# Kernel optimization log

Measured on AMD Instinct MI355X. Metric: run time of the kernel, lower is better.

## Reference

```python
import jax, jax.numpy as jnp
import numpy as np


def setup_inputs() -> dict:
    key = jax.random.key(0)
    k1, k2, k3, k4, k5 = jax.random.split(key, 5)
    B, S, T = 256, 512, 64
    emissions = jax.random.normal(k1, (B, S, T), dtype=jnp.float32)
    tags = jax.random.randint(k2, (B, S), 0, T, dtype=jnp.int64)
    mask = jnp.ones((B, S), dtype=jnp.int32)
    init_range = 0.1
    start_transitions = jax.random.uniform(k3, (T,), minval=-init_range, maxval=init_range, dtype=jnp.float32)
    end_transitions = jax.random.uniform(k4, (T,), minval=-init_range, maxval=init_range, dtype=jnp.float32)
    transitions = jax.random.uniform(k5, (T, T), minval=-init_range, maxval=init_range, dtype=jnp.float32)
    return {"emissions": emissions, "tags": tags, "mask": mask,
            "start_transitions": start_transitions,
            "end_transitions": end_transitions,
            "transitions": transitions}


def _crf_nll_mean(emissions, tags, mask, start_transitions, end_transitions, transitions):
    # batch_first -> time-major: [S, B, T], [S, B]
    em = jnp.transpose(emissions, (1, 0, 2))
    tg = jnp.transpose(tags, (1, 0))
    mk = jnp.transpose(mask, (1, 0))
    maskf = mk.astype(em.dtype)                      # [S, B]
    S, B, T = em.shape
    batch_idx = jnp.arange(B)

    # ---- numerator: score of the gold path (fully vectorized) ----
    emit = jnp.take_along_axis(em, tg[:, :, None], axis=2)[..., 0]   # [S, B]
    trans_sc = transitions[tg[:-1], tg[1:]]                          # [S-1, B]
    score_num = start_transitions[tg[0]] + emit[0]
    score_num = score_num + jnp.sum((trans_sc + emit[1:]) * maskf[1:], axis=0)
    seq_ends = jnp.sum(mk, axis=0) - 1                               # [B]
    last_tags = tg[seq_ends, batch_idx]
    score_num = score_num + end_transitions[last_tags]

    # ---- denominator: log-partition via logsumexp scan ----
    init = start_transitions + em[0]                                 # [B, T]

    def step(score, xs):
        em_i, m_i = xs                                               # [B,T], [B]
        # [B, T_prev, T_next]
        next_score = score[:, :, None] + transitions[None, :, :] + em_i[:, None, :]
        next_score = jax.nn.logsumexp(next_score, axis=1)
        score = jnp.where(m_i[:, None] != 0, next_score, score)
        return score, None

    final, _ = jax.lax.scan(step, init, (em[1:], mk[1:]))
    denom = jax.nn.logsumexp(final + end_transitions, axis=1)        # [B]

    llh = denom - score_num                                          # [B]
    return jnp.mean(llh)                                             # reduction='mean'


def reference(emissions, tags, mask, start_transitions, end_transitions, transitions):
    return _crf_nll_mean(emissions, tags, mask, start_transitions, end_transitions, transitions)
```

## Files before the change

### kernel.cpp

```cpp
#include <hip/hip_runtime.h>

#define BATCH 256
#define SEQ   512
#define NT    64
#define PCH   8
#define CLEN  64
#define PITCH 68

typedef __attribute__((ext_vector_type(8)))  short bf16x8;
typedef __attribute__((ext_vector_type(16))) float f32x16;
typedef __attribute__((ext_vector_type(4)))  float f32x4;

static __device__ __forceinline__ unsigned pk_bf16(float lo, float hi) {
    return (__float_as_uint(hi) & 0xffff0000u) | (__float_as_uint(lo) >> 16);
}
static __device__ __forceinline__ short bf16_trunc(float v) {
    return (short)(__float_as_uint(v) >> 16);
}

__global__ __launch_bounds__(64, 2) void crf_chunk_kernel(
    const float* __restrict__ emissions,
    const float* __restrict__ trans,
    unsigned short* __restrict__ mats,
    float* __restrict__ ws_head)
{
    __shared__ __align__(16) unsigned char smem[CLEN * NT * 4];
    float (*w_lds)[NT] = (float (*)[NT])smem;
    unsigned short* ldsT = (unsigned short*)smem;

    const int c    = blockIdx.x;
    const int b    = blockIdx.y;
    const int lane = threadIdx.x;
    const int h    = lane >> 5;
    const int ml   = lane & 31;

    if (c == 0 && b == 0 && lane == 0) {
        ws_head[0] = 0.f;
        ((unsigned*)ws_head)[1] = 0u;
    }

    const int s0 = c * CLEN;
    int L = (SEQ - 1) - s0; if (L > CLEN) L = CLEN;

    const float* em_b = emissions + (size_t)b * SEQ * NT;
    for (int s = 0; s < L; ++s)
        w_lds[s][lane] = __expf(em_b[(size_t)(s0 + 1 + s) * NT + lane]);

    bf16x8 Af[2][4];
#pragma unroll
    for (int mt = 0; mt < 2; ++mt) {
        int m = mt * 32 + ml;
#pragma unroll
        for (int kk = 0; kk < 4; ++kk) {
            bf16x8 f;
#pragma unroll
            for (int j = 0; j < 8; ++j) {
                int r = 32 * (kk >> 1) + 16 * (kk & 1) + (j & 3) + 8 * (j >> 2) + 4 * h;
                f[j] = bf16_trunc(__expf(trans[r * NT + m]) * 0.0078125f);
            }
            Af[mt][kk] = f;
        }
    }

    union BU { unsigned u[4]; bf16x8 v; };
    BU Bv[4][2];
#pragma unroll
    for (int kk = 0; kk < 4; ++kk)
#pragma unroll
        for (int nt = 0; nt < 2; ++nt) {
            int n = nt * 32 + ml;
#pragma unroll
            for (int d = 0; d < 4; ++d) {
                int j0 = 2 * d;
                int r0 = 32 * (kk >> 1) + 16 * (kk & 1) + (j0 & 3) + 8 * (j0 >> 2) + 4 * h;
                unsigned lo = (r0     == n) ? 0x3f80u : 0u;
                unsigned hi = (r0 + 1 == n) ? 0x3f80u : 0u;
                Bv[kk][nt].u[d] = lo | (hi << 16);
            }
        }

    __threadfence_block();

    const f32x16 zf = {};

    for (int s = 0; s < L; ++s) {
        f32x4 wq[4][2];
#pragma unroll
        for (int kk = 0; kk < 4; ++kk) {
            int base = 32 * (kk >> 1) + 16 * (kk & 1) + 4 * h;
            wq[kk][0] = *(const f32x4*)&w_lds[s][base];
            wq[kk][1] = *(const f32x4*)&w_lds[s][base + 8];
        }

        f32x16 acc[2][2];
#pragma unroll
        for (int mt = 0; mt < 2; ++mt)
#pragma unroll
            for (int nt = 0; nt < 2; ++nt) {
                f32x16 a = __builtin_amdgcn_mfma_f32_32x32x16_bf16(Af[mt][0], Bv[0][nt].v, zf, 0, 0, 0);
                a = __builtin_amdgcn_mfma_f32_32x32x16_bf16(Af[mt][1], Bv[1][nt].v, a, 0, 0, 0);
                a = __builtin_amdgcn_mfma_f32_32x32x16_bf16(Af[mt][2], Bv[2][nt].v, a, 0, 0, 0);
                a = __builtin_amdgcn_mfma_f32_32x32x16_bf16(Af[mt][3], Bv[3][nt].v, a, 0, 0, 0);
                acc[mt][nt] = a;
            }

#pragma unroll
        for (int kk = 0; kk < 4; ++kk) {
            const int mt_s = kk >> 1, qo = 8 * (kk & 1);
#pragma unroll
            for (int nt = 0; nt < 2; ++nt) {
#pragma unroll
                for (int d = 0; d < 4; ++d) {
                    int j0 = 2 * d;
                    float v0 = acc[mt_s][nt][qo + j0]     * wq[kk][j0 >> 2][j0 & 3];
                    float v1 = acc[mt_s][nt][qo + j0 + 1] * wq[kk][(j0 + 1) >> 2][(j0 + 1) & 3];
                    Bv[kk][nt].u[d] = pk_bf16(v0, v1);
                }
            }
        }
    }

    __threadfence_block();
#pragma unroll
    for (int kk = 0; kk < 4; ++kk)
#pragma unroll
        for (int nt = 0; nt < 2; ++nt) {
            int n = nt * 32 + ml;
#pragma unroll
            for (int d = 0; d < 4; ++d) {
                int j0 = 2 * d;
                int r0 = 32 * (kk >> 1) + 16 * (kk & 1) + (j0 & 3) + 8 * (j0 >> 2) + 4 * h;
                *(unsigned*)&ldsT[n * PITCH + r0] = Bv[kk][nt].u[d];
            }
        }
    __threadfence_block();

    unsigned short* outp = mats + ((size_t)(b * PCH + c)) * 4096;
    for (int it = 0; it < 8; ++it) {
        int o = it * 512 + lane * 8;
        int n = o >> 6, k = o & 63;
        const uint2* p = (const uint2*)(ldsT + n * PITCH + k);
        uint2 x = p[0], y = p[1];
        uint4 q4; q4.x = x.x; q4.y = x.y; q4.z = y.x; q4.w = y.y;
        *(uint4*)(outp + o) = q4;
    }
}

__global__ __launch_bounds__(256) void crf_combine_kernel(
    const float* __restrict__ emissions,
    const int*   __restrict__ tags,
    const int*   __restrict__ mask,
    const float* __restrict__ start_tr,
    const float* __restrict__ end_tr,
    const float* __restrict__ trans,
    const unsigned short* __restrict__ mats,
    float* __restrict__ ws_head,
    float* __restrict__ out)
{
    __shared__ __align__(16) float r_lds[NT];
    __shared__ float score_lds;

    const int b    = blockIdx.x;
    const int tid  = threadIdx.x;
    const int j    = tid & 63;
    const int wave = tid >> 6;

    const float* em_b = emissions + (size_t)b * SEQ * NT;
    const int*   tg_b = tags + b * SEQ;
    const int*   mk_b = mask + b * SEQ;
    const unsigned short* mb = mats + (size_t)b * PCH * 4096;

    float denom = 0.f;

    if (wave >= 2) {
        const uint4* p = (const uint4*)mb;
        unsigned acc = 0;
        for (int i = (wave - 2) * 64 + j; i < PCH * 512; i += 128) {
            uint4 q = p[i];
            acc += q.x + q.y + q.z + q.w;
        }
        if (acc == 0xdeadbeefu) ws_head[2] = -1.f;
    } else if (wave == 1) {
        float part = 0.f;
        int mcount = 0;
        for (int s = j; s < SEQ; s += 64) {
            int m = mk_b[s];
            mcount += m;
            int t = tg_b[s];
            if (s == 0) {
                part += start_tr[t] + em_b[t];
            } else {
                int tp = tg_b[s - 1];
                float v = trans[tp * NT + t] + em_b[s * NT + t];
                part += m ? v : 0.f;
            }
        }
#pragma unroll
        for (int d = 32; d; d >>= 1) {
            part   += __shfl_xor(part, d);
            mcount += __shfl_xor(mcount, d);
        }
        if (j == 0) score_lds = part + end_tr[tg_b[mcount - 1]];
    } else {
        float r = __expf(end_tr[j]);
        r_lds[j] = r;
        __threadfence_block();
        int X = 0;

        uint4 cur[8], nxt[8];
#pragma unroll
        for (int u = 0; u < 8; ++u)
            cur[u] = *(const uint4*)(mb + (size_t)(PCH - 1) * 4096 + j * 64 + u * 8);

        for (int c = PCH - 1; c >= 0; --c) {
            if (c > 0) {
#pragma unroll
                for (int u = 0; u < 8; ++u)
                    nxt[u] = *(const uint4*)(mb + (size_t)(c - 1) * 4096 + j * 64 + u * 8);
            }
            float a0 = 0.f, a1 = 0.f, a2 = 0.f, a3 = 0.f;
#pragma unroll
            for (int u = 0; u < 8; ++u) {
                uint4 q = cur[u];
                f32x4 ra = *(const f32x4*)&r_lds[u * 8];
                f32x4 rb = *(const f32x4*)&r_lds[u * 8 + 4];
                a0 = fmaf(ra[0], __uint_as_float(q.x << 16),         a0);
                a1 = fmaf(ra[1], __uint_as_float(q.x & 0xffff0000u), a1);
                a2 = fmaf(ra[2], __uint_as_float(q.y << 16),         a2);
                a3 = fmaf(ra[3], __uint_as_float(q.y & 0xffff0000u), a3);
                a0 = fmaf(rb[0], __uint_as_float(q.z << 16),         a0);
                a1 = fmaf(rb[1], __uint_as_float(q.z & 0xffff0000u), a1);
                a2 = fmaf(rb[2], __uint_as_float(q.w << 16),         a2);
                a3 = fmaf(rb[3], __uint_as_float(q.w & 0xffff0000u), a3);
            }
            float rn = (a0 + a1) + (a2 + a3);
            unsigned eb = (__builtin_amdgcn_readfirstlane((int)__float_as_uint(rn)) >> 23) & 0xffu;
            r = rn * __uint_as_float((254u - eb) << 23);
            X += (int)eb - 127;
            r_lds[j] = r;
            __threadfence_block();
#pragma unroll
            for (int u = 0; u < 8; ++u) cur[u] = nxt[u];
        }

        float u0 = __expf(start_tr[j] + em_b[j]);
        float v = r * u0;
#pragma unroll
        for (int d = 32; d; d >>= 1) v += __shfl_xor(v, d);
        denom = __logf(v) + (float)(X + 7 * (SEQ - 1)) * 0.6931471805599453f;
    }

    __syncthreads();

    if (wave == 0 && j == 0) {
        float llh = denom - score_lds;
        atomicAdd(&ws_head[0], llh * (1.0f / BATCH));
        __threadfence();
        unsigned old = atomicAdd((unsigned*)ws_head + 1, 1u);
        if (old == BATCH - 1) {
            __threadfence();
            out[0] = atomicAdd(&ws_head[0], 0.0f);
        }
    }
}

extern "C" void kernel_launch(void* const* d_in, const int* in_sizes, int n_in,
                              void* d_out, int out_size, void* d_ws, size_t ws_size,
                              hipStream_t stream) {
    const float* emissions = (const float*)d_in[0];
    const int*   tags      = (const int*)d_in[1];
    const int*   mask      = (const int*)d_in[2];
    const float* start_tr  = (const float*)d_in[3];
    const float* end_tr    = (const float*)d_in[4];
    const float* trans     = (const float*)d_in[5];

    float* ws_head = (float*)d_ws;
    unsigned short* mats = (unsigned short*)((char*)d_ws + 4096);

    crf_chunk_kernel<<<dim3(PCH, BATCH), 64, 0, stream>>>(emissions, trans, mats, ws_head);
    crf_combine_kernel<<<BATCH, 256, 0, stream>>>(emissions, tags, mask,
                                                  start_tr, end_tr, trans, mats,
                                                  ws_head, (float*)d_out);
}
```

Baseline: 154.7 us.

## Split sequence into 12 chunks and interleave MFMA with rescale epilogue

Measured after the change: 151.0 us. 1.02x faster.

```diff
diff --git a/kernel.cpp b/kernel.cpp
--- a/kernel.cpp
+++ b/kernel.cpp
@@ -3,30 +3,31 @@
 #define BATCH 256
 #define SEQ   512
 #define NT    64
-#define PCH   8
-#define CLEN  64
 #define PITCH 68
 
 typedef __attribute__((ext_vector_type(8)))  short bf16x8;
 typedef __attribute__((ext_vector_type(16))) float f32x16;
 typedef __attribute__((ext_vector_type(4)))  float f32x4;
+typedef __attribute__((ext_vector_type(2)))  float f32x2;
 
 static __device__ __forceinline__ unsigned pk_bf16(float lo, float hi) {
-    return (__float_as_uint(hi) & 0xffff0000u) | (__float_as_uint(lo) >> 16);
+    return __builtin_amdgcn_perm(__float_as_uint(hi), __float_as_uint(lo), 0x07060302u);
 }
 static __device__ __forceinline__ short bf16_trunc(float v) {
     return (short)(__float_as_uint(v) >> 16);
 }
 
-__global__ __launch_bounds__(64, 2) void crf_chunk_kernel(
+template<int PCH_, int CLEN_>
+__global__ __launch_bounds__(64, 3) void crf_chunk_kernel(
     const float* __restrict__ emissions,
     const float* __restrict__ trans,
     unsigned short* __restrict__ mats,
     float* __restrict__ ws_head)
 {
-    __shared__ __align__(16) unsigned char smem[CLEN * NT * 4];
-    float (*w_lds)[NT] = (float (*)[NT])smem;
-    unsigned short* ldsT = (unsigned short*)smem;
+    constexpr int SMEM = (CLEN_ * NT * 4 > 64 * PITCH * 2) ? CLEN_ * NT * 4 : 64 * PITCH * 2;
+    __shared__ __align__(16) unsigned char smem[SMEM];
+    float*          w_flat = (float*)smem;
+    unsigned short* ldsT   = (unsigned short*)smem;
 
     const int c    = blockIdx.x;
     const int b    = blockIdx.y;
@@ -39,12 +40,22 @@
         ((unsigned*)ws_head)[1] = 0u;
     }
 
-    const int s0 = c * CLEN;
-    int L = (SEQ - 1) - s0; if (L > CLEN) L = CLEN;
+    const int s0 = c * CLEN_;
+    int L = (SEQ - 1) - s0; if (L > CLEN_) L = CLEN_;
 
     const float* em_b = emissions + (size_t)b * SEQ * NT;
-    for (int s = 0; s < L; ++s)
-        w_lds[s][lane] = __expf(em_b[(size_t)(s0 + 1 + s) * NT + lane]);
+
+    {
+        const float4* src = (const float4*)(em_b + (size_t)(s0 + 1) * NT);
+        float4*       dst = (float4*)w_flat;
+        const int total4 = L * (NT / 4);
+        for (int i = lane; i < total4; i += 64) {
+            float4 v = src[i];
+            v.x = __expf(v.x); v.y = __expf(v.y);
+            v.z = __expf(v.z); v.w = __expf(v.w);
+            dst[i] = v;
+        }
+    }
 
     bf16x8 Af[2][4];
 #pragma unroll
@@ -84,37 +95,42 @@
     const f32x16 zf = {};
 
     for (int s = 0; s < L; ++s) {
+        const float* wrow = w_flat + s * NT;
         f32x4 wq[4][2];
 #pragma unroll
         for (int kk = 0; kk < 4; ++kk) {
             int base = 32 * (kk >> 1) + 16 * (kk & 1) + 4 * h;
-            wq[kk][0] = *(const f32x4*)&w_lds[s][base];
-            wq[kk][1] = *(const f32x4*)&w_lds[s][base + 8];
-        }
-
-        f32x16 acc[2][2];
-#pragma unroll
-        for (int mt = 0; mt < 2; ++mt)
-#pragma unroll
-            for (int nt = 0; nt < 2; ++nt) {
-                f32x16 a = __builtin_amdgcn_mfma_f32_32x32x16_bf16(Af[mt][0], Bv[0][nt].v, zf, 0, 0, 0);
-                a = __builtin_amdgcn_mfma_f32_32x32x16_bf16(Af[mt][1], Bv[1][nt].v, a, 0, 0, 0);
-                a = __builtin_amdgcn_mfma_f32_32x32x16_bf16(Af[mt][2], Bv[2][nt].v, a, 0, 0, 0);
-                a = __builtin_amdgcn_mfma_f32_32x32x16_bf16(Af[mt][3], Bv[3][nt].v, a, 0, 0, 0);
-                acc[mt][nt] = a;
-            }
-
-#pragma unroll
-        for (int kk = 0; kk < 4; ++kk) {
-            const int mt_s = kk >> 1, qo = 8 * (kk & 1);
-#pragma unroll
-            for (int nt = 0; nt < 2; ++nt) {
+            wq[kk][0] = *(const f32x4*)(wrow + base);
+            wq[kk][1] = *(const f32x4*)(wrow + base + 8);
+        }
+
+#pragma unroll
+        for (int nt = 0; nt < 2; ++nt) {
+            __builtin_amdgcn_s_setprio(1);
+            f32x16 a0 = __builtin_amdgcn_mfma_f32_32x32x16_bf16(Af[0][0], Bv[0][nt].v, zf, 0, 0, 0);
+            f32x16 a1 = __builtin_amdgcn_mfma_f32_32x32x16_bf16(Af[1][0], Bv[0][nt].v, zf, 0, 0, 0);
+#pragma unroll
+            for (int kk = 1; kk < 4; ++kk) {
+                a0 = __builtin_amdgcn_mfma_f32_32x32x16_bf16(Af[0][kk], Bv[kk][nt].v, a0, 0, 0, 0);
+                a1 = __builtin_amdgcn_mfma_f32_32x32x16_bf16(Af[1][kk], Bv[kk][nt].v, a1, 0, 0, 0);
+            }
+            __builtin_amdgcn_s_setprio(0);
+
+#pragma unroll
+            for (int kk = 0; kk < 4; ++kk) {
+                const int qo = 8 * (kk & 1);
+                const f32x4 wa = wq[kk][0], wb = wq[kk][1];
 #pragma unroll
                 for (int d = 0; d < 4; ++d) {
-                    int j0 = 2 * d;
-                    float v0 = acc[mt_s][nt][qo + j0]     * wq[kk][j0 >> 2][j0 & 3];
-                    float v1 = acc[mt_s][nt][qo + j0 + 1] * wq[kk][(j0 + 1) >> 2][(j0 + 1) & 3];
-                    Bv[kk][nt].u[d] = pk_bf16(v0, v1);
+                    const int j0 = 2 * d;
+                    float w0 = (d < 2) ? wa[j0]     : wb[j0 - 4];
+                    float w1 = (d < 2) ? wa[j0 + 1] : wb[j0 - 3];
+                    f32x2 av, wv;
+                    if (kk < 2) { av[0] = a0[qo + j0]; av[1] = a0[qo + j0 + 1]; }
+                    else        { av[0] = a1[qo + j0]; av[1] = a1[qo + j0 + 1]; }
+                    wv[0] = w0; wv[1] = w1;
+                    f32x2 p = av * wv;
+                    Bv[kk][nt].u[d] = pk_bf16(p[0], p[1]);
                 }
             }
         }
@@ -135,7 +151,7 @@
         }
     __threadfence_block();
 
-    unsigned short* outp = mats + ((size_t)(b * PCH + c)) * 4096;
+    unsigned short* outp = mats + ((size_t)(b * PCH_ + c)) * 4096;
     for (int it = 0; it < 8; ++it) {
         int o = it * 512 + lane * 8;
         int n = o >> 6, k = o & 63;
@@ -146,6 +162,7 @@
     }
 }
 
+template<int PCH_>
 __global__ __launch_bounds__(256) void crf_combine_kernel(
     const float* __restrict__ emissions,
     const int*   __restrict__ tags,
@@ -168,14 +185,14 @@
     const float* em_b = emissions + (size_t)b * SEQ * NT;
     const int*   tg_b = tags + b * SEQ;
     const int*   mk_b = mask + b * SEQ;
-    const unsigned short* mb = mats + (size_t)b * PCH * 4096;
+    const unsigned short* mb = mats + (size_t)b * PCH_ * 4096;
 
     float denom = 0.f;
 
     if (wave >= 2) {
         const uint4* p = (const uint4*)mb;
         unsigned acc = 0;
-        for (int i = (wave - 2) * 64 + j; i < PCH * 512; i += 128) {
+        for (int i = (wave - 2) * 64 + j; i < PCH_ * 512; i += 128) {
             uint4 q = p[i];
             acc += q.x + q.y + q.z + q.w;
         }
@@ -210,9 +227,9 @@
         uint4 cur[8], nxt[8];
 #pragma unroll
         for (int u = 0; u < 8; ++u)
-            cur[u] = *(const uint4*)(mb + (size_t)(PCH - 1) * 4096 + j * 64 + u * 8);
-
-        for (int c = PCH - 1; c >= 0; --c) {
+            cur[u] = *(const uint4*)(mb + (size_t)(PCH_ - 1) * 4096 + j * 64 + u * 8);
+
+        for (int c = PCH_ - 1; c >= 0; --c) {
             if (c > 0) {
 #pragma unroll
                 for (int u = 0; u < 8; ++u)
@@ -277,8 +294,16 @@
     float* ws_head = (float*)d_ws;
     unsigned short* mats = (unsigned short*)((char*)d_ws + 4096);
 
-    crf_chunk_kernel<<<dim3(PCH, BATCH), 64, 0, stream>>>(emissions, trans, mats, ws_head);
-    crf_combine_kernel<<<BATCH, 256, 0, stream>>>(emissions, tags, mask,
-                                                  start_tr, end_tr, trans, mats,
-                                                  ws_head, (float*)d_out);
-}
+    const size_t need12 = 4096 + (size_t)BATCH * 12 * 4096 * sizeof(unsigned short);
+    if (ws_size >= need12) {
+        crf_chunk_kernel<12, 43><<<dim3(12, BATCH), 64, 0, stream>>>(emissions, trans, mats, ws_head);
+        crf_combine_kernel<12><<<BATCH, 256, 0, stream>>>(emissions, tags, mask,
+                                                          start_tr, end_tr, trans, mats,
+                                                          ws_head, (float*)d_out);
+    } else {
+        crf_chunk_kernel<8, 64><<<dim3(8, BATCH), 64, 0, stream>>>(emissions, trans, mats, ws_head);
+        crf_combine_kernel<8><<<BATCH, 256, 0, stream>>>(emissions, tags, mask,
+                                                         start_tr, end_tr, trans, mats,
+                                                         ws_head, (float*)d_out);
+    }
+}
```
